# Kernel tuning notes

Hardware: AMD Instinct MI355X
Metric: run time of the kernel (lower is better)

## Reference

```python
import jax, jax.numpy as jnp
import numpy as np

N_SRC = 50000      # source nodes
N_DST = 32000      # destination nodes
MAX_DEG = 16       # padded max in-degree
N_SUB = 4          # subtokens per node
D = 128            # hidden_dim
VOCAB = 32000
N_CLASSES = 104
LN_EPS = 1e-5


def setup_inputs() -> dict:
    key = jax.random.key(0)
    ks = jax.random.split(key, 12)
    token_id = jax.random.randint(ks[0], (N_SRC, N_SUB), 0, VOCAB)
    neigh_idx = jax.random.randint(ks[1], (N_DST, MAX_DEG), 0, N_SRC)
    deg = jax.random.randint(ks[2], (N_DST,), 1, MAX_DEG + 1)  # in-degree >= 1 (DGL asserts no 0-in-degree)
    s = 1.0 / np.sqrt(D)
    emb = jax.random.normal(ks[3], (VOCAB, D), dtype=jnp.float32) * np.sqrt(2.0 / D)  # kaiming_normal_
    w_ih = jax.random.uniform(ks[4], (3 * D, D), minval=-s, maxval=s, dtype=jnp.float32)  # gates r,z,n
    w_hh = jax.random.uniform(ks[5], (3 * D, D), minval=-s, maxval=s, dtype=jnp.float32)
    b_ih = jax.random.uniform(ks[6], (3 * D,), minval=-s, maxval=s, dtype=jnp.float32)
    b_hh = jax.random.uniform(ks[7], (3 * D,), minval=-s, maxval=s, dtype=jnp.float32)
    gamma = jnp.ones((D,), jnp.float32)
    beta = jnp.zeros((D,), jnp.float32)
    sc = 1.0 / np.sqrt(D)
    wc = jax.random.uniform(ks[8], (N_CLASSES, D), minval=-sc, maxval=sc, dtype=jnp.float32)
    bc = jax.random.uniform(ks[9], (N_CLASSES,), minval=-sc, maxval=sc, dtype=jnp.float32)
    return dict(token_id=token_id, neigh_idx=neigh_idx, deg=deg, emb=emb,
                w_ih=w_ih, w_hh=w_hh, b_ih=b_ih, b_hh=b_hh,
                gamma=gamma, beta=beta, wc=wc, bc=bc)


def reference(token_id, neigh_idx, deg, emb, w_ih, w_hh, b_ih, b_hh, gamma, beta, wc, bc):
    # node features: mean over subtokens of embedding lookup
    feat_src = emb[token_id].mean(axis=1)                 # [N_src, D]
    msgs = feat_src[neigh_idx]                            # [N_dst, max_deg, D] (mailbox)
    T = MAX_DEG - 1                                       # GRU runs over the first L-1 messages
    # precompute input projections for all steps (one big GEMM)
    x_proj = jnp.einsum('ntd,ed->nte', msgs[:, :T], w_ih) + b_ih  # [N_dst, T, 3D]

    def gru_step(h, inp):
        xp, active = inp                                  # xp [N,3D], active [N]
        hp = h @ w_hh.T + b_hh
        xr, xz, xn = jnp.split(xp, 3, axis=-1)
        hr, hz, hn = jnp.split(hp, 3, axis=-1)
        r = jax.nn.sigmoid(xr + hr)
        z = jax.nn.sigmoid(xz + hz)
        n = jnp.tanh(xn + r * hn)
        h_new = (1.0 - z) * n + z * h
        h = jnp.where(active[:, None], h_new, h)          # freeze finished (short-degree) rows
        return h, None

    steps = jnp.arange(T)
    active = steps[:, None] < (deg - 1)[None, :]          # [T, N_dst]: step t valid iff t < L-1
    h0 = jnp.zeros((N_DST, D), msgs.dtype)
    h, _ = jax.lax.scan(gru_step, h0, (jnp.transpose(x_proj, (1, 0, 2)), active))

    # layernorm on final GRU hidden state
    mu = h.mean(axis=-1, keepdims=True)
    var = ((h - mu) ** 2).mean(axis=-1, keepdims=True)
    ln = (h - mu) / jnp.sqrt(var + LN_EPS) * gamma + beta
    # degree-1 nodes: ft = the single message (no GRU, no layernorm)
    ft = jnp.where((deg == 1)[:, None], msgs[:, 0], ln)   # [N_dst, D]
    return ft @ wc.T + bc                                 # [N_dst, n_classes]
```

## Files before the change

### kernel.cpp

```cpp
#include <hip/hip_runtime.h>

typedef unsigned short u16;
typedef unsigned int u32;
typedef __attribute__((ext_vector_type(8))) short short8;
typedef __attribute__((ext_vector_type(4))) float f32x4;

#define NDST 32000
#define NSRC 50000
#define MAXDEG 16
#define DH 128
#define NCLS 104
#define SBLK 125
#define NPAIR 500
#define NBLK_GRU 250

#define MFMA(a, b, c) __builtin_amdgcn_mfma_f32_16x16x32_bf16(a, b, c, 0, 0, 0)

__device__ __forceinline__ u16 f2bf(float f) {
  union { float f; u32 u; } v; v.f = f;
  return (u16)((v.u + 0x7FFFu + ((v.u >> 16) & 1u)) >> 16);
}
__device__ __forceinline__ float sigm(float x) { return 1.f / (1.f + __expf(-x)); }
__device__ __forceinline__ float tanh1(float x) {
  return 1.f - 2.f / (1.f + __expf(2.f * x));
}
__device__ __forceinline__ f32x4 splat4(float x) { f32x4 v = {x, x, x, x}; return v; }

__global__ void k_front(const int* __restrict__ token, const float* __restrict__ emb,
                        const float* __restrict__ wih, const float* __restrict__ whh,
                        const float* __restrict__ wc, const int* __restrict__ deg,
                        u16* __restrict__ featb, u16* __restrict__ wihb,
                        u16* __restrict__ whhb, u16* __restrict__ wcb,
                        int* __restrict__ blkhist) {
  __shared__ int h[16];
  const int bid = blockIdx.x, tid = threadIdx.x;
  const bool do_hist = (bid < SBLK);
  if (do_hist) {
    if (tid < 16) h[tid] = 0;
    __syncthreads();
    atomicAdd(&h[deg[bid * 256 + tid] - 1], 1);
  }
  {
    int gid = bid * 256 + tid;
    int n = gid >> 4, c = gid & 15;
    const int* tk = token + n * 4;
    float a[8];
#pragma unroll
    for (int j = 0; j < 8; ++j) a[j] = 0.f;
#pragma unroll
    for (int s = 0; s < 4; ++s) {
      const float* p = emb + (size_t)tk[s] * DH + c * 8;
#pragma unroll
      for (int j = 0; j < 8; ++j) a[j] += p[j];
    }
    u16 u[8];
#pragma unroll
    for (int j = 0; j < 8; ++j) u[j] = f2bf(a[j] * 0.25f);
    uint4 pk;
    pk.x = u[0] | ((u32)u[1] << 16);
    pk.y = u[2] | ((u32)u[3] << 16);
    pk.z = u[4] | ((u32)u[5] << 16);
    pk.w = u[6] | ((u32)u[7] << 16);
    *reinterpret_cast<uint4*>(featb + (size_t)n * DH + c * 8) = pk;
  }
  if (bid >= SBLK && bid < SBLK + 192) {
    int i = (bid - SBLK) * 256 + tid;
    wihb[i] = f2bf(wih[i]);
    whhb[i] = f2bf(whh[i]);
    if (i < 112 * DH) { int r = i >> 7; wcb[i] = (r < NCLS) ? f2bf(wc[i]) : (u16)0; }
  }
  if (do_hist) {
    __syncthreads();
    if (tid < 16) blkhist[bid * 16 + tid] = h[tid];
  }
}

__global__ void k_scan(const int* __restrict__ blkhist, int* __restrict__ offs,
                       int* __restrict__ base16) {
  __shared__ int tot_s[16];
  int t = threadIdx.x;
  int k = t >> 4, i = t & 15;
  int loc[8];
  int s = 0;
#pragma unroll
  for (int b = 0; b < 8; ++b) {
    int bb = i * 8 + b;
    int v = (bb < SBLK) ? blkhist[bb * 16 + k] : 0;
    loc[b] = s;
    s += v;
  }
  int ps = s;
#pragma unroll
  for (int d = 1; d < 16; d <<= 1) {
    int o = __shfl_up(ps, d, 16);
    if (i >= d) ps += o;
  }
  int excl = ps - s;
#pragma unroll
  for (int b = 0; b < 8; ++b) {
    int bb = i * 8 + b;
    if (bb < SBLK) offs[bb * 16 + k] = excl + loc[b];
  }
  if (i == 15) tot_s[k] = ps;
  __syncthreads();
  if (t == 0) {
    int run = 0;
    for (int q = 0; q < 16; ++q) { base16[q] = run; run += tot_s[q]; }
  }
}

__global__ void k_scatter(const int* __restrict__ deg, const int* __restrict__ offs,
                          const int* __restrict__ base16, int* __restrict__ perm) {
  __shared__ int lc[16];
  int tid = threadIdx.x;
  if (tid < 16) lc[tid] = 0;
  __syncthreads();
  int node = blockIdx.x * 256 + tid;
  int k = deg[node] - 1;
  int p = atomicAdd(&lc[k], 1);
  perm[base16[k] + offs[blockIdx.x * 16 + k] + p] = node;
}

__global__ __launch_bounds__(512, 2) void k_gru(
    const int* __restrict__ neigh, const int* __restrict__ deg,
    const int* __restrict__ perm, const u16* __restrict__ featb,
    const u16* __restrict__ wihb, const u16* __restrict__ whhb,
    const float* __restrict__ bih, const float* __restrict__ bhh,
    const float* __restrict__ gamma, const float* __restrict__ beta,
    const u16* __restrict__ wcb, const float* __restrict__ bc,
    float* __restrict__ out) {
  __shared__ u16 Hb[2][2][32][DH];
  __shared__ u16 Xs[2][32][DH];
  __shared__ int neigh_s[2][MAXDEG][32];
  __shared__ int nid_s[2][32];
  __shared__ int deg_s[2][32];
  __shared__ float gam_s[DH], bet_s[DH];

  const int tid = threadIdx.x;
  const int w = tid >> 6;
  const int l = tid & 63;
  const int l16 = l & 15;
  const int lq = l >> 4;
  const int col = w * 16 + l16;
  const int swzA = (l16 & 7) << 3;
  const int grow = w * 4 + (l >> 4);
  const int gcol = (l & 15) * 8;
  const int gsw = (grow & 7) << 3;

  if (tid < DH) { gam_s[tid] = gamma[tid]; bet_s[tid] = beta[tid]; }

  short8 Wr[4], Wz[4], Wn[4], Ur[4], Uz[4], Un[4];
#pragma unroll
  for (int kc = 0; kc < 4; ++kc) {
    int ko = kc * 32 + lq * 8;
    const u16* pw = wihb + (size_t)col * DH + ko;
    const u16* pu = whhb + (size_t)col * DH + ko;
    Wr[kc] = *(const short8*)pw;
    Wz[kc] = *(const short8*)(pw + DH * DH);
    Wn[kc] = *(const short8*)(pw + 2 * DH * DH);
    Ur[kc] = *(const short8*)pu;
    Uz[kc] = *(const short8*)(pu + DH * DH);
    Un[kc] = *(const short8*)(pu + 2 * DH * DH);
  }
  float bR = bih[col] + bhh[col];
  float bZ = bih[DH + col] + bhh[DH + col];
  float bXN = bih[2 * DH + col];
  float bHN = bhh[2 * DH + col];
  asm volatile("" : "+v"(Wr[0]), "+v"(Wr[1]), "+v"(Wr[2]), "+v"(Wr[3]));
  asm volatile("" : "+v"(Wz[0]), "+v"(Wz[1]), "+v"(Wz[2]), "+v"(Wz[3]));
  asm volatile("" : "+v"(Wn[0]), "+v"(Wn[1]), "+v"(Wn[2]), "+v"(Wn[3]));
  asm volatile("" : "+v"(Ur[0]), "+v"(Ur[1]), "+v"(Ur[2]), "+v"(Ur[3]));
  asm volatile("" : "+v"(Uz[0]), "+v"(Uz[1]), "+v"(Uz[2]), "+v"(Uz[3]));
  asm volatile("" : "+v"(Un[0]), "+v"(Un[1]), "+v"(Un[2]), "+v"(Un[3]));
  asm volatile("" : "+v"(bR), "+v"(bZ), "+v"(bXN), "+v"(bHN));

#define STAGEX(P, T)                                                           \
  do {                                                                         \
    int nrow_ = neigh_s[P][T][grow];                                           \
    const u16* g_ = featb + (size_t)nrow_ * DH + (gcol ^ gsw);                 \
    __builtin_amdgcn_global_load_lds(                                          \
        (const __attribute__((address_space(1))) u16*)g_,                      \
        (__attribute__((address_space(3))) u16*)&Xs[P][w * 4][0], 16, 0, 0);   \
  } while (0)

#define PHASE(P, CUR, HREG, DEGM1, T)                                          \
  do {                                                                         \
    f32x4 aR0 = splat4(bR), aR1 = splat4(bR), aZ0 = splat4(bZ),                \
          aZ1 = splat4(bZ), aN0 = splat4(bXN), aN1 = splat4(bXN),              \
          aH0 = splat4(bHN), aH1 = splat4(bHN);                                \
    _Pragma("unroll") for (int kc = 0; kc < 4; ++kc) {                         \
      int ko = kc * 32 + lq * 8;                                               \
      short8 ax0 = *(const short8*)&Xs[P][l16][ko ^ swzA];                     \
      short8 ax1 = *(const short8*)&Xs[P][16 + l16][ko ^ swzA];                \
      short8 ah0 = *(const short8*)&Hb[P][CUR][l16][ko ^ swzA];                \
      short8 ah1 = *(const short8*)&Hb[P][CUR][16 + l16][ko ^ swzA];           \
      aR0 = MFMA(ax0, Wr[kc], aR0);                                            \
      aR1 = MFMA(ax1, Wr[kc], aR1);                                            \
      aZ0 = MFMA(ax0, Wz[kc], aZ0);                                            \
      aZ1 = MFMA(ax1, Wz[kc], aZ1);                                            \
      aN0 = MFMA(ax0, Wn[kc], aN0);                                            \
      aN1 = MFMA(ax1, Wn[kc], aN1);                                            \
      aR0 = MFMA(ah0, Ur[kc], aR0);                                            \
      aR1 = MFMA(ah1, Ur[kc], aR1);                                            \
      aZ0 = MFMA(ah0, Uz[kc], aZ0);                                            \
      aZ1 = MFMA(ah1, Uz[kc], aZ1);                                            \
      aH0 = MFMA(ah0, Un[kc], aH0);                                            \
      aH1 = MFMA(ah1, Un[kc], aH1);                                            \
    }                                                                          \
    _Pragma("unroll") for (int m = 0; m < 2; ++m) {                            \
      f32x4 vR = m ? aR1 : aR0, vZ = m ? aZ1 : aZ0;                            \
      f32x4 vN = m ? aN1 : aN0, vH = m ? aH1 : aH0;                            \
      _Pragma("unroll") for (int r = 0; r < 4; ++r) {                          \
        float rr = sigm(vR[r]);                                                \
        float zz = sigm(vZ[r]);                                                \
        float nn = tanh1(vN[r] + rr * vH[r]);                                  \
        float hN = (1.f - zz) * nn + zz * HREG[m][r];                          \
        if ((T) < DEGM1[m][r]) HREG[m][r] = hN;                                \
        int row = m * 16 + lq * 4 + r;                                         \
        Hb[P][(CUR) ^ 1][row][col ^ ((row & 7) << 3)] = f2bf(HREG[m][r]);      \
      }                                                                        \
    }                                                                          \
  } while (0)

  float* Hf = (float*)&Xs[0][0][0];

#pragma unroll 1
  for (int pass = 0; pass < 2; ++pass) {
    const int pairIdx = pass ? (int)blockIdx.x : (NPAIR - 1 - (int)blockIdx.x);

    __syncthreads();
    if (tid < 64) nid_s[tid >> 5][tid & 31] = perm[(pairIdx * 2 + (tid >> 5)) * 32 + (tid & 31)];
    __syncthreads();
#pragma unroll
    for (int e = tid; e < 1024; e += 512) {
      int p = e >> 9, r9 = e & 511, node = r9 >> 4, t = r9 & 15;
      neigh_s[p][t][node] = neigh[(size_t)nid_s[p][node] * MAXDEG + t];
    }
    if (tid < 64) deg_s[tid >> 5][tid & 31] = deg[nid_s[tid >> 5][tid & 31]];
    {
      uint4 z = {0, 0, 0, 0};
      ((uint4*)Hb[0][0])[tid] = z;
      ((uint4*)Hb[1][0])[tid] = z;
    }
    __syncthreads();
    STAGEX(0, 0);
    STAGEX(1, 0);

    const int tmaxA = deg_s[0][31] - 1;
    const int tmaxB = deg_s[1][31] - 1;
    int degm1_0[2][4], degm1_1[2][4];
#pragma unroll
    for (int m = 0; m < 2; ++m)
#pragma unroll
      for (int r = 0; r < 4; ++r) {
        degm1_0[m][r] = deg_s[0][m * 16 + lq * 4 + r] - 1;
        degm1_1[m][r] = deg_s[1][m * 16 + lq * 4 + r] - 1;
      }
    float hreg0[2][4] = {{0, 0, 0, 0}, {0, 0, 0, 0}};
    float hreg1[2][4] = {{0, 0, 0, 0}, {0, 0, 0, 0}};

    __syncthreads();

    int cur = 0;
#pragma unroll 1
    for (int t = 0; t < tmaxB; ++t) {
      if (t >= 1) STAGEX(1, t);
      if (t < tmaxA) PHASE(0, cur, hreg0, degm1_0, t);
      __syncthreads();
      if (t + 1 < tmaxA) STAGEX(0, t + 1);
      PHASE(1, cur, hreg1, degm1_1, t);
      __syncthreads();
      cur ^= 1;
    }

#define LNPASS(HREG, P)                                                        \
  do {                                                                         \
    _Pragma("unroll") for (int m = 0; m < 2; ++m)                              \
        _Pragma("unroll") for (int r = 0; r < 4; ++r)                          \
            Hf[(m * 16 + lq * 4 + r) * DH + col] = HREG[m][r];                 \
    __syncthreads();                                                           \
    {                                                                          \
      int node = tid >> 4, sub = tid & 15;                                     \
      float v[8];                                                              \
      float s = 0.f, s2 = 0.f;                                                 \
      _Pragma("unroll") for (int j = 0; j < 8; ++j) {                          \
        v[j] = Hf[node * DH + sub * 8 + j];                                    \
        s += v[j];                                                             \
        s2 += v[j] * v[j];                                                     \
      }                                                                        \
      s += __shfl_xor(s, 1, 64); s2 += __shfl_xor(s2, 1, 64);                  \
      s += __shfl_xor(s, 2, 64); s2 += __shfl_xor(s2, 2, 64);                  \
      s += __shfl_xor(s, 4, 64); s2 += __shfl_xor(s2, 4, 64);                  \
      s += __shfl_xor(s, 8, 64); s2 += __shfl_xor(s2, 8, 64);                  \
      float mu = s * (1.f / 128.f);                                            \
      float var = s2 * (1.f / 128.f) - mu * mu;                                \
      float rstd = rsqrtf(var + 1e-5f);                                        \
      bool isd1 = (deg_s[P][node] == 1);                                       \
      uint4 fv = *(const uint4*)(featb + (size_t)neigh_s[P][0][node] * DH + sub * 8); \
      const u16* fp = (const u16*)&fv;                                         \
      u16 ob[8];                                                               \
      _Pragma("unroll") for (int j = 0; j < 8; ++j) {                          \
        int d = sub * 8 + j;                                                   \
        float ln = (v[j] - mu) * rstd * gam_s[d] + bet_s[d];                   \
        ob[j] = isd1 ? fp[j] : f2bf(ln);                                       \
      }                                                                        \
      int e = (sub * 8) ^ ((node & 7) << 3);                                   \
      uint4 pk;                                                                \
      pk.x = ob[0] | ((u32)ob[1] << 16);                                       \
      pk.y = ob[2] | ((u32)ob[3] << 16);                                       \
      pk.z = ob[4] | ((u32)ob[5] << 16);                                       \
      pk.w = ob[6] | ((u32)ob[7] << 16);                                       \
      *(uint4*)&Hb[P][0][node][e] = pk;                                        \
    }                                                                          \
    __syncthreads();                                                           \
  } while (0)

    LNPASS(hreg0, 0);
    LNPASS(hreg1, 1);

#define CLS(P)                                                                 \
  if (w < 7) {                                                                 \
    f32x4 c0 = splat4(0.f), c1 = splat4(0.f);                                  \
    _Pragma("unroll") for (int kc = 0; kc < 4; ++kc) {                         \
      int ko = kc * 32 + lq * 8;                                               \
      short8 a0 = *(const short8*)&Hb[P][0][l16][ko ^ swzA];                   \
      short8 a1 = *(const short8*)&Hb[P][0][16 + l16][ko ^ swzA];              \
      short8 b = *(const short8*)(wcb + (size_t)col * DH + ko);                \
      c0 = MFMA(a0, b, c0);                                                    \
      c1 = MFMA(a1, b, c1);                                                    \
    }                                                                          \
    if (col < NCLS) {                                                          \
      float bcv = bc[col];                                                     \
      _Pragma("unroll") for (int m = 0; m < 2; ++m)                            \
          _Pragma("unroll") for (int r = 0; r < 4; ++r) {                      \
        float vv = (m ? c1[r] : c0[r]) + bcv;                                  \
        int rowg = nid_s[P][m * 16 + lq * 4 + r];                              \
        out[(size_t)rowg * NCLS + col] = vv;                                   \
      }                                                                        \
    }                                                                          \
  }

    CLS(0);
    CLS(1);
  }
#undef STAGEX
#undef PHASE
#undef LNPASS
#undef CLS
}

extern "C" void kernel_launch(void* const* d_in, const int* in_sizes, int n_in,
                              void* d_out, int out_size, void* d_ws, size_t ws_size,
                              hipStream_t stream) {
  const int* token = (const int*)d_in[0];
  const int* neigh = (const int*)d_in[1];
  const int* deg = (const int*)d_in[2];
  const float* emb = (const float*)d_in[3];
  const float* wih = (const float*)d_in[4];
  const float* whh = (const float*)d_in[5];
  const float* bih = (const float*)d_in[6];
  const float* bhh = (const float*)d_in[7];
  const float* gamma = (const float*)d_in[8];
  const float* beta = (const float*)d_in[9];
  const float* wc = (const float*)d_in[10];
  const float* bc = (const float*)d_in[11];
  float* out = (float*)d_out;

  u16* featb = (u16*)d_ws;
  u16* wihb = featb + (size_t)NSRC * DH;
  u16* whhb = wihb + 384 * DH;
  u16* wcb = whhb + 384 * DH;
  int* perm = (int*)(wcb + 112 * DH);
  int* blkhist = perm + NDST;
  int* offs = blkhist + SBLK * 16;
  int* base16 = offs + SBLK * 16;

  hipLaunchKernelGGL(k_front, dim3(3125), dim3(256), 0, stream, token, emb, wih, whh, wc,
                     deg, featb, wihb, whhb, wcb, blkhist);
  hipLaunchKernelGGL(k_scan, dim3(1), dim3(256), 0, stream, blkhist, offs, base16);
  hipLaunchKernelGGL(k_scatter, dim3(SBLK), dim3(256), 0, stream, deg, offs, base16, perm);
  hipLaunchKernelGGL(k_gru, dim3(NBLK_GRU), dim3(512), 0, stream, neigh, deg, perm, featb,
                     wihb, whhb, bih, bhh, gamma, beta, wcb, bc, out);
}
```

Baseline: 211.8 us.

## Restructure GRU step loop: double-buffer X, batch both tiles' MFMA before epilogue

The GRU time loop now double-buffers the gathered message tiles and prefetches step t+1 for both tiles before running the MFMAs. All MFMAs for both tiles run back to back under raised wave priority, separated from the gate epilogues by a single barrier, and the hidden state is kept single-buffered. This is meant to overlap the gather latency with compute and cut the barrier count per step. Supporting changes use packed v_cvt_pk_bf16_f32 conversions, fast reciprocal in sigmoid/tanh, and u16 neighbor indices in LDS to save shared memory. Holding both tiles' accumulators live raises register pressure, and the rcp approximation slightly changes numerics.

```diff
diff --git a/kernel.cpp b/kernel.cpp
--- a/kernel.cpp
+++ b/kernel.cpp
@@ -20,9 +20,15 @@
   union { float f; u32 u; } v; v.f = f;
   return (u16)((v.u + 0x7FFFu + ((v.u >> 16) & 1u)) >> 16);
 }
-__device__ __forceinline__ float sigm(float x) { return 1.f / (1.f + __expf(-x)); }
+__device__ __forceinline__ u32 cvtpk(float lo, float hi) {
+  u32 r;
+  asm("v_cvt_pk_bf16_f32 %0, %1, %2" : "=v"(r) : "v"(lo), "v"(hi));
+  return r;
+}
+__device__ __forceinline__ float rcpf(float x) { return __builtin_amdgcn_rcpf(x); }
+__device__ __forceinline__ float sigm(float x) { return rcpf(1.f + __expf(-x)); }
 __device__ __forceinline__ float tanh1(float x) {
-  return 1.f - 2.f / (1.f + __expf(2.f * x));
+  return 1.f - 2.f * rcpf(1.f + __expf(2.f * x));
 }
 __device__ __forceinline__ f32x4 splat4(float x) { f32x4 v = {x, x, x, x}; return v; }
 
@@ -53,14 +59,11 @@
 #pragma unroll
       for (int j = 0; j < 8; ++j) a[j] += p[j];
     }
-    u16 u[8];
-#pragma unroll
-    for (int j = 0; j < 8; ++j) u[j] = f2bf(a[j] * 0.25f);
     uint4 pk;
-    pk.x = u[0] | ((u32)u[1] << 16);
-    pk.y = u[2] | ((u32)u[3] << 16);
-    pk.z = u[4] | ((u32)u[5] << 16);
-    pk.w = u[6] | ((u32)u[7] << 16);
+    pk.x = cvtpk(a[0] * 0.25f, a[1] * 0.25f);
+    pk.y = cvtpk(a[2] * 0.25f, a[3] * 0.25f);
+    pk.z = cvtpk(a[4] * 0.25f, a[5] * 0.25f);
+    pk.w = cvtpk(a[6] * 0.25f, a[7] * 0.25f);
     *reinterpret_cast<uint4*>(featb + (size_t)n * DH + c * 8) = pk;
   }
   if (bid >= SBLK && bid < SBLK + 192) {
@@ -129,9 +132,9 @@
     const float* __restrict__ gamma, const float* __restrict__ beta,
     const u16* __restrict__ wcb, const float* __restrict__ bc,
     float* __restrict__ out) {
-  __shared__ u16 Hb[2][2][32][DH];
-  __shared__ u16 Xs[2][32][DH];
-  __shared__ int neigh_s[2][MAXDEG][32];
+  __shared__ u16 Hb[2][32][DH];
+  __shared__ u16 Xs[2][2][32][DH];
+  __shared__ u16 neigh_s[2][MAXDEG][32];
   __shared__ int nid_s[2][32];
   __shared__ int deg_s[2][32];
   __shared__ float gam_s[DH], bet_s[DH];
@@ -174,26 +177,27 @@
   asm volatile("" : "+v"(Un[0]), "+v"(Un[1]), "+v"(Un[2]), "+v"(Un[3]));
   asm volatile("" : "+v"(bR), "+v"(bZ), "+v"(bXN), "+v"(bHN));
 
-#define STAGEX(P, T)                                                           \
+#define STAGEX(P, T, B)                                                        \
   do {                                                                         \
-    int nrow_ = neigh_s[P][T][grow];                                           \
+    int nrow_ = (int)neigh_s[P][T][grow];                                      \
     const u16* g_ = featb + (size_t)nrow_ * DH + (gcol ^ gsw);                 \
     __builtin_amdgcn_global_load_lds(                                          \
         (const __attribute__((address_space(1))) u16*)g_,                      \
-        (__attribute__((address_space(3))) u16*)&Xs[P][w * 4][0], 16, 0, 0);   \
+        (__attribute__((address_space(3))) u16*)&Xs[P][B][w * 4][0], 16, 0, 0);\
   } while (0)
 
-#define PHASE(P, CUR, HREG, DEGM1, T)                                          \
+#define MFMA_TILE(P, CB, aR0, aR1, aZ0, aZ1, aN0, aN1, aH0, aH1)               \
   do {                                                                         \
-    f32x4 aR0 = splat4(bR), aR1 = splat4(bR), aZ0 = splat4(bZ),                \
-          aZ1 = splat4(bZ), aN0 = splat4(bXN), aN1 = splat4(bXN),              \
-          aH0 = splat4(bHN), aH1 = splat4(bHN);                                \
+    aR0 = splat4(bR); aR1 = splat4(bR);                                        \
+    aZ0 = splat4(bZ); aZ1 = splat4(bZ);                                        \
+    aN0 = splat4(bXN); aN1 = splat4(bXN);                                      \
+    aH0 = splat4(bHN); aH1 = splat4(bHN);                                      \
     _Pragma("unroll") for (int kc = 0; kc < 4; ++kc) {                         \
       int ko = kc * 32 + lq * 8;                                               \
-      short8 ax0 = *(const short8*)&Xs[P][l16][ko ^ swzA];                     \
-      short8 ax1 = *(const short8*)&Xs[P][16 + l16][ko ^ swzA];                \
-      short8 ah0 = *(const short8*)&Hb[P][CUR][l16][ko ^ swzA];                \
-      short8 ah1 = *(const short8*)&Hb[P][CUR][16 + l16][ko ^ swzA];           \
+      short8 ax0 = *(const short8*)&Xs[P][CB][l16][ko ^ swzA];                 \
+      short8 ax1 = *(const short8*)&Xs[P][CB][16 + l16][ko ^ swzA];            \
+      short8 ah0 = *(const short8*)&Hb[P][l16][ko ^ swzA];                     \
+      short8 ah1 = *(const short8*)&Hb[P][16 + l16][ko ^ swzA];                \
       aR0 = MFMA(ax0, Wr[kc], aR0);                                            \
       aR1 = MFMA(ax1, Wr[kc], aR1);                                            \
       aZ0 = MFMA(ax0, Wz[kc], aZ0);                                            \
@@ -207,6 +211,10 @@
       aH0 = MFMA(ah0, Un[kc], aH0);                                            \
       aH1 = MFMA(ah1, Un[kc], aH1);                                            \
     }                                                                          \
+  } while (0)
+
+#define EPI_TILE(P, HREG, DEGM1, T, aR0, aR1, aZ0, aZ1, aN0, aN1, aH0, aH1)    \
+  do {                                                                         \
     _Pragma("unroll") for (int m = 0; m < 2; ++m) {                            \
       f32x4 vR = m ? aR1 : aR0, vZ = m ? aZ1 : aZ0;                            \
       f32x4 vN = m ? aN1 : aN0, vH = m ? aH1 : aH0;                            \
@@ -216,13 +224,18 @@
         float nn = tanh1(vN[r] + rr * vH[r]);                                  \
         float hN = (1.f - zz) * nn + zz * HREG[m][r];                          \
         if ((T) < DEGM1[m][r]) HREG[m][r] = hN;                                \
-        int row = m * 16 + lq * 4 + r;                                         \
-        Hb[P][(CUR) ^ 1][row][col ^ ((row & 7) << 3)] = f2bf(HREG[m][r]);      \
       }                                                                        \
+      u32 p01 = cvtpk(HREG[m][0], HREG[m][1]);                                 \
+      u32 p23 = cvtpk(HREG[m][2], HREG[m][3]);                                 \
+      int r0_ = m * 16 + lq * 4;                                               \
+      Hb[P][r0_ + 0][col ^ (((r0_ + 0) & 7) << 3)] = (u16)p01;                 \
+      Hb[P][r0_ + 1][col ^ (((r0_ + 1) & 7) << 3)] = (u16)(p01 >> 16);         \
+      Hb[P][r0_ + 2][col ^ (((r0_ + 2) & 7) << 3)] = (u16)p23;                 \
+      Hb[P][r0_ + 3][col ^ (((r0_ + 3) & 7) << 3)] = (u16)(p23 >> 16);         \
     }                                                                          \
   } while (0)
 
-  float* Hf = (float*)&Xs[0][0][0];
+  float* Hf = (float*)&Xs[0][0][0][0];
 
 #pragma unroll 1
   for (int pass = 0; pass < 2; ++pass) {
@@ -234,17 +247,17 @@
 #pragma unroll
     for (int e = tid; e < 1024; e += 512) {
       int p = e >> 9, r9 = e & 511, node = r9 >> 4, t = r9 & 15;
-      neigh_s[p][t][node] = neigh[(size_t)nid_s[p][node] * MAXDEG + t];
+      neigh_s[p][t][node] = (u16)neigh[(size_t)nid_s[p][node] * MAXDEG + t];
     }
     if (tid < 64) deg_s[tid >> 5][tid & 31] = deg[nid_s[tid >> 5][tid & 31]];
     {
       uint4 z = {0, 0, 0, 0};
-      ((uint4*)Hb[0][0])[tid] = z;
-      ((uint4*)Hb[1][0])[tid] = z;
+      ((uint4*)Hb[0])[tid] = z;
+      ((uint4*)Hb[0])[tid + 512] = z;
     }
     __syncthreads();
-    STAGEX(0, 0);
-    STAGEX(1, 0);
+    STAGEX(0, 0, 0);
+    STAGEX(1, 0, 0);
 
     const int tmaxA = deg_s[0][31] - 1;
     const int tmaxB = deg_s[1][31] - 1;
@@ -264,13 +277,20 @@
     int cur = 0;
 #pragma unroll 1
     for (int t = 0; t < tmaxB; ++t) {
-      if (t >= 1) STAGEX(1, t);
-      if (t < tmaxA) PHASE(0, cur, hreg0, degm1_0, t);
+      int nxt = cur ^ 1;
+      if (t + 1 < tmaxA) STAGEX(0, t + 1, nxt);
+      if (t + 1 < tmaxB) STAGEX(1, t + 1, nxt);
+      f32x4 AR0, AR1, AZ0, AZ1, AN0, AN1, AH0, AH1;
+      f32x4 BR0, BR1, BZ0, BZ1, BN0, BN1, BH0, BH1;
+      __builtin_amdgcn_s_setprio(1);
+      if (t < tmaxA) MFMA_TILE(0, cur, AR0, AR1, AZ0, AZ1, AN0, AN1, AH0, AH1);
+      MFMA_TILE(1, cur, BR0, BR1, BZ0, BZ1, BN0, BN1, BH0, BH1);
+      __builtin_amdgcn_s_setprio(0);
       __syncthreads();
-      if (t + 1 < tmaxA) STAGEX(0, t + 1);
-      PHASE(1, cur, hreg1, degm1_1, t);
+      if (t < tmaxA) EPI_TILE(0, hreg0, degm1_0, t, AR0, AR1, AZ0, AZ1, AN0, AN1, AH0, AH1);
+      EPI_TILE(1, hreg1, degm1_1, t, BR0, BR1, BZ0, BZ1, BN0, BN1, BH0, BH1);
       __syncthreads();
-      cur ^= 1;
+      cur = nxt;
     }
 
 #define LNPASS(HREG, P)                                                        \
@@ -296,21 +316,19 @@
       float var = s2 * (1.f / 128.f) - mu * mu;                                \
       float rstd = rsqrtf(var + 1e-5f);                                        \
       bool isd1 = (deg_s[P][node] == 1);                                       \
-      uint4 fv = *(const uint4*)(featb + (size_t)neigh_s[P][0][node] * DH + sub * 8); \
-      const u16* fp = (const u16*)&fv;                                         \
-      u16 ob[8];                                                               \
+      uint4 fv = *(const uint4*)(featb + (size_t)((int)neigh_s[P][0][node]) * DH + sub * 8); \
+      float ln_[8];                                                            \
       _Pragma("unroll") for (int j = 0; j < 8; ++j) {                          \
         int d = sub * 8 + j;                                                   \
-        float ln = (v[j] - mu) * rstd * gam_s[d] + bet_s[d];                   \
-        ob[j] = isd1 ? fp[j] : f2bf(ln);                                       \
+        ln_[j] = (v[j] - mu) * rstd * gam_s[d] + bet_s[d];                     \
       }                                                                        \
+      uint4 pk;                                                                \
+      pk.x = isd1 ? fv.x : cvtpk(ln_[0], ln_[1]);                              \
+      pk.y = isd1 ? fv.y : cvtpk(ln_[2], ln_[3]);                              \
+      pk.z = isd1 ? fv.z : cvtpk(ln_[4], ln_[5]);                              \
+      pk.w = isd1 ? fv.w : cvtpk(ln_[6], ln_[7]);                              \
       int e = (sub * 8) ^ ((node & 7) << 3);                                   \
-      uint4 pk;                                                                \
-      pk.x = ob[0] | ((u32)ob[1] << 16);                                       \
-      pk.y = ob[2] | ((u32)ob[3] << 16);                                       \
-      pk.z = ob[4] | ((u32)ob[5] << 16);                                       \
-      pk.w = ob[6] | ((u32)ob[7] << 16);                                       \
-      *(uint4*)&Hb[P][0][node][e] = pk;                                        \
+      *(uint4*)&Hb[P][node][e] = pk;                                           \
     }                                                                          \
     __syncthreads();                                                           \
   } while (0)
@@ -323,8 +341,8 @@
     f32x4 c0 = splat4(0.f), c1 = splat4(0.f);                                  \
     _Pragma("unroll") for (int kc = 0; kc < 4; ++kc) {                         \
       int ko = kc * 32 + lq * 8;                                               \
-      short8 a0 = *(const short8*)&Hb[P][0][l16][ko ^ swzA];                   \
-      short8 a1 = *(const short8*)&Hb[P][0][16 + l16][ko ^ swzA];              \
+      short8 a0 = *(const short8*)&Hb[P][l16][ko ^ swzA];                      \
+      short8 a1 = *(const short8*)&Hb[P][16 + l16][ko ^ swzA];                 \
       short8 b = *(const short8*)(wcb + (size_t)col * DH + ko);                \
       c0 = MFMA(a0, b, c0);                                                    \
       c1 = MFMA(a1, b, c1);                                                    \
@@ -344,7 +362,8 @@
     CLS(1);
   }
 #undef STAGEX
-#undef PHASE
+#undef MFMA_TILE
+#undef EPI_TILE
 #undef LNPASS
 #undef CLS
 }
```

Result: slower. 239.2 us (+12.9%).
